# Optimization experiments

Measured on AMD Instinct MI355X. Metric: run time of the kernel, lower is better.

The kernel has to match this reference:

```python
import jax, jax.numpy as jnp
import numpy as np

EMBED_DIM = 1024
N1 = 4096
N2 = 4096


def setup_inputs() -> dict:
    key = jax.random.key(0)
    ks = jax.random.split(key, 14)
    s = 1.0 / np.sqrt(EMBED_DIM)
    def lin(k):
        kw, kb = jax.random.split(k)
        W = jax.random.uniform(kw, (EMBED_DIM, EMBED_DIM), jnp.float32, -s, s)
        b = jax.random.uniform(kb, (EMBED_DIM,), jnp.float32, -s, s)
        return W, b
    Wq1, bq1 = lin(ks[0]); Wk1, bk1 = lin(ks[1]); Wv1, bv1 = lin(ks[2])
    Wq2, bq2 = lin(ks[3]); Wk2, bk2 = lin(ks[4]); Wv2, bv2 = lin(ks[5])
    x1 = jax.random.normal(ks[6], (N1, EMBED_DIM), jnp.float32)
    x2 = jax.random.normal(ks[7], (N2, EMBED_DIM), jnp.float32)
    return {
        "input_tensor1": x1, "input_tensor2": x2,
        "Wq1": Wq1, "bq1": bq1, "Wk1": Wk1, "bk1": bk1, "Wv1": Wv1, "bv1": bv1,
        "Wq2": Wq2, "bq2": bq2, "Wk2": Wk2, "bk2": bk2, "Wv2": Wv2, "bv2": bv2,
    }


def reference(input_tensor1, input_tensor2,
              Wq1, bq1, Wk1, bk1, Wv1, bv1,
              Wq2, bq2, Wk2, bk2, Wv2, bv2):
    scale = 1.0 / jnp.sqrt(jnp.asarray(EMBED_DIM, input_tensor1.dtype))
    # torch Linear: y = x @ W.T + b
    q1 = input_tensor1 @ Wq1.T + bq1   # [N1, D]
    k1 = input_tensor1 @ Wk1.T + bk1
    v1 = input_tensor1 @ Wv1.T + bv1
    q2 = input_tensor2 @ Wq2.T + bq2   # [N2, D]
    k2 = input_tensor2 @ Wk2.T + bk2
    v2 = input_tensor2 @ Wv2.T + bv2
    # stream-2 queries attend over stream-1 keys/values
    scores1 = (q2 @ k1.T) * scale                  # [N2, N1]
    probs1 = jax.nn.softmax(scores1, axis=-1)      # dropout p=0 -> identity
    context1 = probs1 @ v1                         # [N2, D]
    # stream-1 queries attend over stream-2 keys/values
    scores2 = (q1 @ k2.T) * scale                  # [N1, N2]
    probs2 = jax.nn.softmax(scores2, axis=-1)
    context2 = probs2 @ v2                         # [N1, D]
    return (context1, context2)
```

## Files before the change

### kernel.cpp

```cpp
#include <hip/hip_runtime.h>
#include <hip/hip_bf16.h>
#include <cstdint>
#include <cstddef>

#define DEVINL __device__ __forceinline__

typedef __attribute__((ext_vector_type(4))) float   f32x4;
typedef __bf16 bf16x8 __attribute__((ext_vector_type(8)));
typedef __attribute__((ext_vector_type(4))) short   short4v;
typedef __attribute__((ext_vector_type(4))) float   float4v;

static constexpr int DIM = 1024;
static constexpr int NTOK = 4096;

DEVINL unsigned short f2bf(float f) {
  unsigned u = __float_as_uint(f);
  u += 0x7FFF + ((u >> 16) & 1);
  return (unsigned short)(u >> 16);
}
DEVINL float bf2f(unsigned short s) {
  return __uint_as_float(((unsigned)s) << 16);
}

DEVINL void gll16(const void* g, void* l) {
  __builtin_amdgcn_global_load_lds(
      (const __attribute__((address_space(1))) void*)g,
      (__attribute__((address_space(3))) void*)l, 16, 0, 0);
}

struct B3 { int bx, by, bz; };
DEVINL B3 xcd_remap(int GX, int GY, int GZ) {
  const int flat = blockIdx.x + GX * (blockIdx.y + GY * blockIdx.z);
  const int nwg  = GX * GY * GZ;
  const int chunk = nwg >> 3;
  const int vbid = (flat & 7) * chunk + (flat >> 3);
  B3 r;
  r.bx = vbid % GX;
  r.by = (vbid / GX) % GY;
  r.bz = vbid / (GX * GY);
  return r;
}

DEVINL void core256x128(const unsigned short* __restrict__ A, int lda,
                        const unsigned short* __restrict__ B, int ldb,
                        int K, int brow, int bcol, f32x4 acc[4][4])
{
  __shared__ unsigned short lds[24576];
  const int t = threadIdx.x;
  const int w = t >> 6, l = t & 63;
  const int wr = w >> 1, wc = w & 1;
  const int l15 = l & 15;
  const int scol = ((l & 3) ^ ((l >> 3) & 3)) << 3;
  const int cs = (((l >> 4) ^ ((l15 >> 1) & 3)) << 3);

  const unsigned short* aL = A + (size_t)(brow * 256 + (l >> 2)) * lda + scol;
  const unsigned short* bL = B + (size_t)(bcol * 128 + (l >> 2)) * ldb + scol;

#pragma unroll
  for (int m = 0; m < 4; ++m)
#pragma unroll
    for (int n = 0; n < 4; ++n) {
      f32x4 z = {0.f, 0.f, 0.f, 0.f};
      acc[m][n] = z;
    }

#define STAGE(buf, kt)                                                         \
  {                                                                            \
    gll16(aL + (size_t)(w * 16) * lda + (size_t)(kt) * 32,                     \
          lds + (buf) * 12288 + w * 512);                                      \
    gll16(aL + (size_t)(128 + w * 16) * lda + (size_t)(kt) * 32,               \
          lds + (buf) * 12288 + 4096 + w * 512);                               \
    gll16(bL + (size_t)(w * 16) * ldb + (size_t)(kt) * 32,                     \
          lds + (buf) * 12288 + 8192 + w * 512);                               \
  }

#define BARR() do { asm volatile("" ::: "memory");                             \
                    __builtin_amdgcn_s_barrier();                              \
                    asm volatile("" ::: "memory"); } while (0)

  const int NT = K >> 5;

  STAGE(0, 0);
  asm volatile("s_waitcnt vmcnt(0)" ::: "memory");
  BARR();

  bf16x8 af[4], bfv[4];
  for (int kt = 0; kt < NT; ++kt) {
    const int cur = kt & 1;
    if (kt + 1 < NT) STAGE(cur ^ 1, kt + 1);

#pragma unroll
    for (int m = 0; m < 4; ++m)
      af[m] = *(const bf16x8*)(lds + cur * 12288 + (wr * 64 + m * 16 + l15) * 32 + cs);
#pragma unroll
    for (int n = 0; n < 4; ++n)
      bfv[n] = *(const bf16x8*)(lds + cur * 12288 + 8192 + (wc * 64 + n * 16 + l15) * 32 + cs);

    __builtin_amdgcn_s_setprio(1);
#pragma unroll
    for (int m = 0; m < 4; ++m)
#pragma unroll
      for (int n = 0; n < 4; ++n)
        acc[m][n] = __builtin_amdgcn_mfma_f32_16x16x32_bf16(af[m], bfv[n], acc[m][n], 0, 0, 0);
    __builtin_amdgcn_s_setprio(0);

    asm volatile("s_waitcnt vmcnt(0)" ::: "memory");
    BARR();
  }
#undef STAGE
#undef BARR
}

__global__ __launch_bounds__(512, 4)
void gemm_scores(const unsigned short* __restrict__ A,
                 const unsigned short* __restrict__ B,
                 unsigned short* __restrict__ S, float scale)
{
  const B3 b = xcd_remap(32, 16, 1);
  f32x4 acc[4][4];
  core256x128(A, DIM, B, DIM, DIM, b.by, b.bx, acc);

  const int t = threadIdx.x, w = t >> 6, l = t & 63;
  const int wr = w >> 1, wc = w & 1;
  const int rr = (l >> 4) * 4, cc = l & 15;
#pragma unroll
  for (int m = 0; m < 4; ++m) {
    const int row0 = b.by * 256 + wr * 64 + m * 16 + rr;
#pragma unroll
    for (int n = 0; n < 4; ++n) {
      const int col = b.bx * 128 + wc * 64 + n * 16 + cc;
#pragma unroll
      for (int i = 0; i < 4; ++i)
        S[(size_t)(row0 + i) * NTOK + col] = f2bf(acc[m][n][i] * scale);
    }
  }
}

__global__ __launch_bounds__(512, 4)
void qkv_gemm(const unsigned short* __restrict__ x1, const unsigned short* __restrict__ x2,
              const unsigned short* __restrict__ W6,
              const float* bq1, const float* bk1, const float* bv1,
              const float* bq2, const float* bk2, const float* bv2,
              unsigned short* q1, unsigned short* k1, unsigned short* v1T,
              unsigned short* q2, unsigned short* k2, unsigned short* v2T)
{
  const B3 b = xcd_remap(8, 16, 6);
  const int g = b.bz;
  const unsigned short* A = (g < 3) ? x1 : x2;
  const unsigned short* W = W6 + (size_t)g * (DIM * DIM);
  const float* bias = (g == 0) ? bq1 : (g == 1) ? bk1 : (g == 2) ? bv1
                    : (g == 3) ? bq2 : (g == 4) ? bk2 : bv2;
  unsigned short* out = (g == 0) ? q1 : (g == 1) ? k1 : (g == 2) ? v1T
                      : (g == 3) ? q2 : (g == 4) ? k2 : v2T;
  const bool vT = (g == 2 || g == 5);

  f32x4 acc[4][4];
  core256x128(A, DIM, W, DIM, DIM, b.by, b.bx, acc);

  const int t = threadIdx.x, w = t >> 6, l = t & 63;
  const int wr = w >> 1, wc = w & 1;
  const int rr = (l >> 4) * 4, cc = l & 15;

  if (!vT) {
#pragma unroll
    for (int m = 0; m < 4; ++m) {
      const int row0 = b.by * 256 + wr * 64 + m * 16 + rr;
#pragma unroll
      for (int n = 0; n < 4; ++n) {
        const int col = b.bx * 128 + wc * 64 + n * 16 + cc;
        const float bv_ = bias[col];
#pragma unroll
        for (int i = 0; i < 4; ++i)
          out[(size_t)(row0 + i) * DIM + col] = f2bf(acc[m][n][i] + bv_);
      }
    }
  } else {
#pragma unroll
    for (int m = 0; m < 4; ++m) {
      const int row0 = b.by * 256 + wr * 64 + m * 16 + rr;
#pragma unroll
      for (int n = 0; n < 4; ++n) {
        const int col = b.bx * 128 + wc * 64 + n * 16 + cc;
        const float bv_ = bias[col];
        short4v pk;
#pragma unroll
        for (int i = 0; i < 4; ++i) pk[i] = (short)f2bf(acc[m][n][i] + bv_);
        *(short4v*)(out + (size_t)col * NTOK + row0) = pk;
      }
    }
  }
}

__global__ __launch_bounds__(512, 4)
void pv_gemm(const unsigned short* __restrict__ S1,
             const unsigned short* __restrict__ S2,
             const unsigned short* __restrict__ vTcat,
             float* __restrict__ out, float* __restrict__ P)
{
  const B3 b = xcd_remap(16, 16, 2);
  const int bx = b.bx, by = b.by, z = b.bz;
  const unsigned short* A = ((bx < 8) ? S1 : S2) + (size_t)z * 2048;
  const unsigned short* B = vTcat + (size_t)z * 2048;

  f32x4 acc[4][4];
  core256x128(A, NTOK, B, NTOK, 2048, by, bx, acc);

  const int t = threadIdx.x, w = t >> 6, l = t & 63;
  const int wr = w >> 1, wc = w & 1;
  const int rr = (l >> 4) * 4, cc = l & 15;
#pragma unroll
  for (int m = 0; m < 4; ++m) {
    const int row0 = by * 256 + wr * 64 + m * 16 + rr;
#pragma unroll
    for (int n = 0; n < 4; ++n) {
      const int cg = bx * 128 + wc * 64 + n * 16 + cc;
#pragma unroll
      for (int i = 0; i < 4; ++i) {
        const int r = row0 + i;
        if (z) {
          P[(size_t)r * 2048 + cg] = acc[m][n][i];
        } else {
          float* dst = (cg < 1024) ? (out + (size_t)r * 1024 + cg)
                                   : (out + 4194304 + (size_t)r * 1024 + (cg - 1024));
          *dst = acc[m][n][i];
        }
      }
    }
  }
}

__global__ __launch_bounds__(256)
void add_pv(float* __restrict__ out, const float* __restrict__ P)
{
  const int idx = blockIdx.x * 256 + threadIdx.x;
  const int r  = idx >> 9;
  const int c4 = (idx & 511) << 2;
  const float4v p = *(const float4v*)(P + (size_t)r * 2048 + c4);
  float* dst = (c4 < 1024) ? (out + (size_t)r * 1024 + c4)
                           : (out + 4194304 + (size_t)r * 1024 + (c4 - 1024));
  float4v a = *(const float4v*)dst;
#pragma unroll
  for (int j = 0; j < 4; ++j) a[j] += p[j];
  *(float4v*)dst = a;
}

__global__ __launch_bounds__(256)
void softmax_inplace(unsigned short* __restrict__ S)
{
  const int row = blockIdx.x;
  unsigned short* r = S + (size_t)row * NTOK;
  const int t = threadIdx.x, wave = t >> 6, lane = t & 63;
  __shared__ float red[4];

  bf16x8 d0 = *(const bf16x8*)(r + t * 8);
  bf16x8 d1 = *(const bf16x8*)(r + 2048 + t * 8);
  float v[16];
  {
    const unsigned short* p0 = (const unsigned short*)&d0;
    const unsigned short* p1 = (const unsigned short*)&d1;
#pragma unroll
    for (int j = 0; j < 8; ++j) { v[j] = bf2f(p0[j]); v[8 + j] = bf2f(p1[j]); }
  }
  float mx = v[0];
#pragma unroll
  for (int j = 1; j < 16; ++j) mx = fmaxf(mx, v[j]);
#pragma unroll
  for (int o = 32; o > 0; o >>= 1) mx = fmaxf(mx, __shfl_xor(mx, o));
  if (lane == 0) red[wave] = mx;
  __syncthreads();
  mx = fmaxf(fmaxf(red[0], red[1]), fmaxf(red[2], red[3]));

  float s = 0.f;
#pragma unroll
  for (int j = 0; j < 16; ++j) { v[j] = __expf(v[j] - mx); s += v[j]; }
#pragma unroll
  for (int o = 32; o > 0; o >>= 1) s += __shfl_xor(s, o);
  __syncthreads();
  if (lane == 0) red[wave] = s;
  __syncthreads();
  s = red[0] + red[1] + red[2] + red[3];
  const float inv = 1.0f / s;

  unsigned short o0[8], o1[8];
#pragma unroll
  for (int j = 0; j < 8; ++j) { o0[j] = f2bf(v[j] * inv); o1[j] = f2bf(v[8 + j] * inv); }
  *(bf16x8*)(r + t * 8)        = *(const bf16x8*)o0;
  *(bf16x8*)(r + 2048 + t * 8) = *(const bf16x8*)o1;
}

__global__ __launch_bounds__(256)
void cvt2(const float* __restrict__ a, const float* __restrict__ b,
          unsigned short* __restrict__ oa, unsigned short* __restrict__ ob)
{
  const float* in = blockIdx.y ? b : a;
  unsigned short* out = blockIdx.y ? ob : oa;
  const size_t i = ((size_t)blockIdx.x * 256 + threadIdx.x) * 4;
  float4v x = *(const float4v*)(in + i);
  short4v o;
#pragma unroll
  for (int j = 0; j < 4; ++j) o[j] = (short)f2bf(x[j]);
  *(short4v*)(out + i) = o;
}

__global__ __launch_bounds__(256)
void cvt_w(const float* w0, const float* w1, const float* w2,
           const float* w3, const float* w4, const float* w5,
           unsigned short* __restrict__ W6)
{
  const float* srcs[6] = {w0, w1, w2, w3, w4, w5};
  const float* in = srcs[blockIdx.y];
  unsigned short* out = W6 + (size_t)blockIdx.y * (DIM * DIM);
  const size_t i = ((size_t)blockIdx.x * 256 + threadIdx.x) * 4;
  float4v x = *(const float4v*)(in + i);
  short4v o;
#pragma unroll
  for (int j = 0; j < 4; ++j) o[j] = (short)f2bf(x[j]);
  *(short4v*)(out + i) = o;
}

extern "C" void kernel_launch(void* const* d_in, const int* in_sizes, int n_in,
                              void* d_out, int out_size, void* d_ws, size_t ws_size,
                              hipStream_t stream)
{
  const float* x1  = (const float*)d_in[0];
  const float* x2  = (const float*)d_in[1];
  const float* Wq1 = (const float*)d_in[2];  const float* bq1 = (const float*)d_in[3];
  const float* Wk1 = (const float*)d_in[4];  const float* bk1 = (const float*)d_in[5];
  const float* Wv1 = (const float*)d_in[6];  const float* bv1 = (const float*)d_in[7];
  const float* Wq2 = (const float*)d_in[8];  const float* bq2 = (const float*)d_in[9];
  const float* Wk2 = (const float*)d_in[10]; const float* bk2 = (const float*)d_in[11];
  const float* Wv2 = (const float*)d_in[12]; const float* bv2 = (const float*)d_in[13];
  float* out = (float*)d_out;

  unsigned short* ws  = (unsigned short*)d_ws;
  const size_t NTD = (size_t)NTOK * DIM;
  const size_t SM  = (size_t)NTOK * NTOK;
  unsigned short* x1b = ws;
  unsigned short* x2b = x1b + NTD;
  unsigned short* W6  = x2b + NTD;
  unsigned short* S1  = ws;
  unsigned short* S2  = ws + SM;
  unsigned short* q1  = ws + 2 * SM;
  unsigned short* k1  = q1 + NTD;
  unsigned short* q2  = k1 + NTD;
  unsigned short* k2  = q2 + NTD;
  unsigned short* vT  = k2 + NTD;
  unsigned short* v1T = vT;
  unsigned short* v2T = vT + NTD;
  float* P = (float*)q1;

  const dim3 blk(256);
  cvt2 <<<dim3(NTD / 1024, 2), blk, 0, stream>>>(x1, x2, x1b, x2b);
  cvt_w<<<dim3((DIM * DIM) / 1024, 6), blk, 0, stream>>>(Wq1, Wk1, Wv1, Wq2, Wk2, Wv2, W6);

  qkv_gemm<<<dim3(8, 16, 6), dim3(512), 0, stream>>>(
      x1b, x2b, W6, bq1, bk1, bv1, bq2, bk2, bv2, q1, k1, v1T, q2, k2, v2T);

  const float scale = 0.03125f;

  gemm_scores<<<dim3(32, 16), dim3(512), 0, stream>>>(q2, k1, S1, scale);
  softmax_inplace<<<dim3(NTOK), blk, 0, stream>>>(S1);
  gemm_scores<<<dim3(32, 16), dim3(512), 0, stream>>>(q1, k2, S2, scale);
  softmax_inplace<<<dim3(NTOK), blk, 0, stream>>>(S2);

  pv_gemm<<<dim3(16, 16, 2), dim3(512), 0, stream>>>(S1, S2, vT, out, P);
  add_pv<<<dim3(8192), blk, 0, stream>>>(out, P);
}
```

Before: 275.7 us.

## Deepen GEMM LDS pipeline to six buffers and drop split-K in PV GEMM

The shared GEMM core moves from double buffering to a six-slot LDS ring with four tiles prefetched ahead. It uses graded vmcnt waits and a single barrier per iteration, so global loads overlap more MFMA work. Launch bounds drop to 2 blocks per SM to fit the larger LDS footprint. The PV GEMM no longer splits K into two halves, which removes the partial-sum buffer and the separate add kernel. The cost is half as many PV blocks and lower occupancy.

Result: no change. 277.0 us (median of 2 runs) (+0.5%).

```diff
diff --git a/kernel.cpp b/kernel.cpp
--- a/kernel.cpp
+++ b/kernel.cpp
@@ -45,16 +45,16 @@
                         const unsigned short* __restrict__ B, int ldb,
                         int K, int brow, int bcol, f32x4 acc[4][4])
 {
-  __shared__ unsigned short lds[24576];
+  __shared__ unsigned short lds[73728];
   const int t = threadIdx.x;
   const int w = t >> 6, l = t & 63;
   const int wr = w >> 1, wc = w & 1;
   const int l15 = l & 15;
   const int scol = ((l & 3) ^ ((l >> 3) & 3)) << 3;
-  const int cs = (((l >> 4) ^ ((l15 >> 1) & 3)) << 3);
-
-  const unsigned short* aL = A + (size_t)(brow * 256 + (l >> 2)) * lda + scol;
-  const unsigned short* bL = B + (size_t)(bcol * 128 + (l >> 2)) * ldb + scol;
+  const int cs   = (((l >> 4) ^ ((l15 >> 1) & 3)) << 3);
+
+  const unsigned short* aL = A + (size_t)(brow * 256 + w * 16 + (l >> 2)) * lda + scol;
+  const unsigned short* bL = B + (size_t)(bcol * 128 + w * 16 + (l >> 2)) * ldb + scol;
 
 #pragma unroll
   for (int m = 0; m < 4; ++m)
@@ -66,35 +66,41 @@
 
 #define STAGE(buf, kt)                                                         \
   {                                                                            \
-    gll16(aL + (size_t)(w * 16) * lda + (size_t)(kt) * 32,                     \
+    gll16(aL + (size_t)(kt) * 32,                                              \
           lds + (buf) * 12288 + w * 512);                                      \
-    gll16(aL + (size_t)(128 + w * 16) * lda + (size_t)(kt) * 32,               \
+    gll16(aL + (size_t)128 * lda + (size_t)(kt) * 32,                          \
           lds + (buf) * 12288 + 4096 + w * 512);                               \
-    gll16(bL + (size_t)(w * 16) * ldb + (size_t)(kt) * 32,                     \
+    gll16(bL + (size_t)(kt) * 32,                                              \
           lds + (buf) * 12288 + 8192 + w * 512);                               \
   }
 
-#define BARR() do { asm volatile("" ::: "memory");                             \
-                    __builtin_amdgcn_s_barrier();                              \
-                    asm volatile("" ::: "memory"); } while (0)
-
   const int NT = K >> 5;
 
-  STAGE(0, 0);
-  asm volatile("s_waitcnt vmcnt(0)" ::: "memory");
-  BARR();
+  STAGE(0, 0); STAGE(1, 1); STAGE(2, 2); STAGE(3, 3);
 
   bf16x8 af[4], bfv[4];
+  int cur = 0;
   for (int kt = 0; kt < NT; ++kt) {
-    const int cur = kt & 1;
-    if (kt + 1 < NT) STAGE(cur ^ 1, kt + 1);
-
+    int st = cur + 4; if (st >= 6) st -= 6;
+    if (kt + 4 < NT) STAGE(st, kt + 4);
+
+    const int rem = NT - 1 - kt;
+    if (rem >= 4)      asm volatile("s_waitcnt vmcnt(12)" ::: "memory");
+    else if (rem == 3) asm volatile("s_waitcnt vmcnt(9)"  ::: "memory");
+    else if (rem == 2) asm volatile("s_waitcnt vmcnt(6)"  ::: "memory");
+    else if (rem == 1) asm volatile("s_waitcnt vmcnt(3)"  ::: "memory");
+    else               asm volatile("s_waitcnt vmcnt(0)"  ::: "memory");
+    asm volatile("" ::: "memory");
+    __builtin_amdgcn_s_barrier();
+    asm volatile("" ::: "memory");
+
+    const unsigned short* base = lds + cur * 12288;
 #pragma unroll
     for (int m = 0; m < 4; ++m)
-      af[m] = *(const bf16x8*)(lds + cur * 12288 + (wr * 64 + m * 16 + l15) * 32 + cs);
+      af[m] = *(const bf16x8*)(base + (wr * 64 + m * 16 + l15) * 32 + cs);
 #pragma unroll
     for (int n = 0; n < 4; ++n)
-      bfv[n] = *(const bf16x8*)(lds + cur * 12288 + 8192 + (wc * 64 + n * 16 + l15) * 32 + cs);
+      bfv[n] = *(const bf16x8*)(base + 8192 + (wc * 64 + n * 16 + l15) * 32 + cs);
 
     __builtin_amdgcn_s_setprio(1);
 #pragma unroll
@@ -104,14 +110,12 @@
         acc[m][n] = __builtin_amdgcn_mfma_f32_16x16x32_bf16(af[m], bfv[n], acc[m][n], 0, 0, 0);
     __builtin_amdgcn_s_setprio(0);
 
-    asm volatile("s_waitcnt vmcnt(0)" ::: "memory");
-    BARR();
+    cur = (cur + 1 == 6) ? 0 : cur + 1;
   }
 #undef STAGE
-#undef BARR
-}
-
-__global__ __launch_bounds__(512, 4)
+}
+
+__global__ __launch_bounds__(512, 2)
 void gemm_scores(const unsigned short* __restrict__ A,
                  const unsigned short* __restrict__ B,
                  unsigned short* __restrict__ S, float scale)
@@ -136,7 +140,7 @@
   }
 }
 
-__global__ __launch_bounds__(512, 4)
+__global__ __launch_bounds__(512, 2)
 void qkv_gemm(const unsigned short* __restrict__ x1, const unsigned short* __restrict__ x2,
               const unsigned short* __restrict__ W6,
               const float* bq1, const float* bk1, const float* bv1,
@@ -191,19 +195,18 @@
   }
 }
 
-__global__ __launch_bounds__(512, 4)
+__global__ __launch_bounds__(512, 2)
 void pv_gemm(const unsigned short* __restrict__ S1,
              const unsigned short* __restrict__ S2,
              const unsigned short* __restrict__ vTcat,
-             float* __restrict__ out, float* __restrict__ P)
-{
-  const B3 b = xcd_remap(16, 16, 2);
-  const int bx = b.bx, by = b.by, z = b.bz;
-  const unsigned short* A = ((bx < 8) ? S1 : S2) + (size_t)z * 2048;
-  const unsigned short* B = vTcat + (size_t)z * 2048;
+             float* __restrict__ out)
+{
+  const B3 b = xcd_remap(16, 16, 1);
+  const int bx = b.bx, by = b.by;
+  const unsigned short* A = (bx < 8) ? S1 : S2;
 
   f32x4 acc[4][4];
-  core256x128(A, NTOK, B, NTOK, 2048, by, bx, acc);
+  core256x128(A, NTOK, vTcat, NTOK, NTOK, by, bx, acc);
 
   const int t = threadIdx.x, w = t >> 6, l = t & 63;
   const int wr = w >> 1, wc = w & 1;
@@ -214,34 +217,12 @@
 #pragma unroll
     for (int n = 0; n < 4; ++n) {
       const int cg = bx * 128 + wc * 64 + n * 16 + cc;
-#pragma unroll
-      for (int i = 0; i < 4; ++i) {
-        const int r = row0 + i;
-        if (z) {
-          P[(size_t)r * 2048 + cg] = acc[m][n][i];
-        } else {
-          float* dst = (cg < 1024) ? (out + (size_t)r * 1024 + cg)
-                                   : (out + 4194304 + (size_t)r * 1024 + (cg - 1024));
-          *dst = acc[m][n][i];
-        }
-      }
-    }
-  }
-}
-
-__global__ __launch_bounds__(256)
-void add_pv(float* __restrict__ out, const float* __restrict__ P)
-{
-  const int idx = blockIdx.x * 256 + threadIdx.x;
-  const int r  = idx >> 9;
-  const int c4 = (idx & 511) << 2;
-  const float4v p = *(const float4v*)(P + (size_t)r * 2048 + c4);
-  float* dst = (c4 < 1024) ? (out + (size_t)r * 1024 + c4)
-                           : (out + 4194304 + (size_t)r * 1024 + (c4 - 1024));
-  float4v a = *(const float4v*)dst;
-#pragma unroll
-  for (int j = 0; j < 4; ++j) a[j] += p[j];
-  *(float4v*)dst = a;
+      float* dstBase = (cg < 1024) ? (out + cg) : (out + 4194304 + (cg - 1024));
+#pragma unroll
+      for (int i = 0; i < 4; ++i)
+        dstBase[(size_t)(row0 + i) * 1024] = acc[m][n][i];
+    }
+  }
 }
 
 __global__ __launch_bounds__(256)
@@ -347,7 +328,6 @@
   unsigned short* vT  = k2 + NTD;
   unsigned short* v1T = vT;
   unsigned short* v2T = vT + NTD;
-  float* P = (float*)q1;
 
   const dim3 blk(256);
   cvt2 <<<dim3(NTD / 1024, 2), blk, 0, stream>>>(x1, x2, x1b, x2b);
@@ -363,6 +343,5 @@
   gemm_scores<<<dim3(32, 16), dim3(512), 0, stream>>>(q1, k2, S2, scale);
   softmax_inplace<<<dim3(NTOK), blk, 0, stream>>>(S2);
 
-  pv_gemm<<<dim3(16, 16, 2), dim3(512), 0, stream>>>(S1, S2, vT, out, P);
-  add_pv<<<dim3(8192), blk, 0, stream>>>(out, P);
-}
+  pv_gemm<<<dim3(16, 16), dim3(512), 0, stream>>>(S1, S2, vT, out);
+}
```

## Use 256x256 GEMM tiles with a four-buffer, three-stage-ahead load pipeline

Applied to the files above, without the earlier changes.

Replaces the 256x128 GEMM core with a 256x256 tile core. Each wave now covers a 128x64 sub-tile (8x4 MFMAs), which raises data reuse per LDS load. The double-buffered loop, which drained all loads with vmcnt(0) on every iteration, becomes a 4-slot ring buffer that prefetches three K-steps ahead and uses partial vmcnt waits. The cost is 128KB of LDS and more accumulator registers per block, so occupancy drops to one block per CU. Grids also halve, leaving fewer blocks than CUs for the scores and PV GEMMs.

Result: faster. 270.0 us (-2.1%).

```diff
diff --git a/kernel.cpp b/kernel.cpp
--- a/kernel.cpp
+++ b/kernel.cpp
@@ -41,23 +41,23 @@
   return r;
 }
 
-DEVINL void core256x128(const unsigned short* __restrict__ A, int lda,
-                        const unsigned short* __restrict__ B, int ldb,
-                        int K, int brow, int bcol, f32x4 acc[4][4])
-{
-  __shared__ unsigned short lds[24576];
+DEVINL void core256sq(const unsigned short* __restrict__ A, int lda,
+                      const unsigned short* __restrict__ B, int ldb,
+                      int K, int brow, int bcol, f32x4 acc[8][4])
+{
+  __shared__ unsigned short lds[65536];
   const int t = threadIdx.x;
   const int w = t >> 6, l = t & 63;
-  const int wr = w >> 1, wc = w & 1;
+  const int wr = w >> 2, wc = w & 3;
   const int l15 = l & 15;
   const int scol = ((l & 3) ^ ((l >> 3) & 3)) << 3;
-  const int cs = (((l >> 4) ^ ((l15 >> 1) & 3)) << 3);
-
-  const unsigned short* aL = A + (size_t)(brow * 256 + (l >> 2)) * lda + scol;
-  const unsigned short* bL = B + (size_t)(bcol * 128 + (l >> 2)) * ldb + scol;
-
-#pragma unroll
-  for (int m = 0; m < 4; ++m)
+  const int cs   = (((l >> 4) ^ ((l15 >> 1) & 3)) << 3);
+
+  const unsigned short* aL = A + (size_t)(brow * 256 + w * 16 + (l >> 2)) * lda + scol;
+  const unsigned short* bL = B + (size_t)(bcol * 256 + w * 16 + (l >> 2)) * ldb + scol;
+
+#pragma unroll
+  for (int m = 0; m < 8; ++m)
 #pragma unroll
     for (int n = 0; n < 4; ++n) {
       f32x4 z = {0.f, 0.f, 0.f, 0.f};
@@ -66,69 +66,69 @@
 
 #define STAGE(buf, kt)                                                         \
   {                                                                            \
-    gll16(aL + (size_t)(w * 16) * lda + (size_t)(kt) * 32,                     \
-          lds + (buf) * 12288 + w * 512);                                      \
-    gll16(aL + (size_t)(128 + w * 16) * lda + (size_t)(kt) * 32,               \
-          lds + (buf) * 12288 + 4096 + w * 512);                               \
-    gll16(bL + (size_t)(w * 16) * ldb + (size_t)(kt) * 32,                     \
-          lds + (buf) * 12288 + 8192 + w * 512);                               \
-  }
-
-#define BARR() do { asm volatile("" ::: "memory");                             \
-                    __builtin_amdgcn_s_barrier();                              \
-                    asm volatile("" ::: "memory"); } while (0)
+    gll16(aL + (size_t)(kt) * 32,                                              \
+          lds + (buf) * 16384 + w * 512);                                      \
+    gll16(aL + (size_t)128 * lda + (size_t)(kt) * 32,                          \
+          lds + (buf) * 16384 + 4096 + w * 512);                               \
+    gll16(bL + (size_t)(kt) * 32,                                              \
+          lds + (buf) * 16384 + 8192 + w * 512);                               \
+    gll16(bL + (size_t)128 * ldb + (size_t)(kt) * 32,                          \
+          lds + (buf) * 16384 + 12288 + w * 512);                              \
+  }
 
   const int NT = K >> 5;
 
-  STAGE(0, 0);
-  asm volatile("s_waitcnt vmcnt(0)" ::: "memory");
-  BARR();
-
-  bf16x8 af[4], bfv[4];
+  STAGE(0, 0); STAGE(1, 1); STAGE(2, 2);
+
+  bf16x8 af[8], bfv[4];
   for (int kt = 0; kt < NT; ++kt) {
-    const int cur = kt & 1;
-    if (kt + 1 < NT) STAGE(cur ^ 1, kt + 1);
-
-#pragma unroll
-    for (int m = 0; m < 4; ++m)
-      af[m] = *(const bf16x8*)(lds + cur * 12288 + (wr * 64 + m * 16 + l15) * 32 + cs);
+    const int rem = NT - 1 - kt;
+    if (rem >= 2)      asm volatile("s_waitcnt vmcnt(8)" ::: "memory");
+    else if (rem == 1) asm volatile("s_waitcnt vmcnt(4)" ::: "memory");
+    else               asm volatile("s_waitcnt vmcnt(0)" ::: "memory");
+    asm volatile("" ::: "memory");
+    __builtin_amdgcn_s_barrier();
+    asm volatile("" ::: "memory");
+
+    if (kt + 3 < NT) STAGE((kt + 3) & 3, kt + 3);
+
+    const unsigned short* base = lds + (kt & 3) * 16384;
+#pragma unroll
+    for (int m = 0; m < 8; ++m)
+      af[m] = *(const bf16x8*)(base + (wr * 128 + m * 16 + l15) * 32 + cs);
 #pragma unroll
     for (int n = 0; n < 4; ++n)
-      bfv[n] = *(const bf16x8*)(lds + cur * 12288 + 8192 + (wc * 64 + n * 16 + l15) * 32 + cs);
+      bfv[n] = *(const bf16x8*)(base + 8192 + (wc * 64 + n * 16 + l15) * 32 + cs);
 
     __builtin_amdgcn_s_setprio(1);
 #pragma unroll
-    for (int m = 0; m < 4; ++m)
+    for (int m = 0; m < 8; ++m)
 #pragma unroll
       for (int n = 0; n < 4; ++n)
         acc[m][n] = __builtin_amdgcn_mfma_f32_16x16x32_bf16(af[m], bfv[n], acc[m][n], 0, 0, 0);
     __builtin_amdgcn_s_setprio(0);
-
-    asm volatile("s_waitcnt vmcnt(0)" ::: "memory");
-    BARR();
   }
 #undef STAGE
-#undef BARR
-}
-
-__global__ __launch_bounds__(512, 4)
+}
+
+__global__ __launch_bounds__(512, 1)
 void gemm_scores(const unsigned short* __restrict__ A,
                  const unsigned short* __restrict__ B,
                  unsigned short* __restrict__ S, float scale)
 {
-  const B3 b = xcd_remap(32, 16, 1);
-  f32x4 acc[4][4];
-  core256x128(A, DIM, B, DIM, DIM, b.by, b.bx, acc);
+  const B3 b = xcd_remap(16, 16, 1);
+  f32x4 acc[8][4];
+  core256sq(A, DIM, B, DIM, DIM, b.by, b.bx, acc);
 
   const int t = threadIdx.x, w = t >> 6, l = t & 63;
-  const int wr = w >> 1, wc = w & 1;
+  const int wr = w >> 2, wc = w & 3;
   const int rr = (l >> 4) * 4, cc = l & 15;
 #pragma unroll
-  for (int m = 0; m < 4; ++m) {
-    const int row0 = b.by * 256 + wr * 64 + m * 16 + rr;
+  for (int m = 0; m < 8; ++m) {
+    const int row0 = b.by * 256 + wr * 128 + m * 16 + rr;
 #pragma unroll
     for (int n = 0; n < 4; ++n) {
-      const int col = b.bx * 128 + wc * 64 + n * 16 + cc;
+      const int col = b.bx * 256 + wc * 64 + n * 16 + cc;
 #pragma unroll
       for (int i = 0; i < 4; ++i)
         S[(size_t)(row0 + i) * NTOK + col] = f2bf(acc[m][n][i] * scale);
@@ -136,7 +136,7 @@
   }
 }
 
-__global__ __launch_bounds__(512, 4)
+__global__ __launch_bounds__(512, 1)
 void qkv_gemm(const unsigned short* __restrict__ x1, const unsigned short* __restrict__ x2,
               const unsigned short* __restrict__ W6,
               const float* bq1, const float* bk1, const float* bv1,
@@ -144,7 +144,7 @@
               unsigned short* q1, unsigned short* k1, unsigned short* v1T,
               unsigned short* q2, unsigned short* k2, unsigned short* v2T)
 {
-  const B3 b = xcd_remap(8, 16, 6);
+  const B3 b = xcd_remap(4, 16, 6);
   const int g = b.bz;
   const unsigned short* A = (g < 3) ? x1 : x2;
   const unsigned short* W = W6 + (size_t)g * (DIM * DIM);
@@ -154,20 +154,20 @@
                       : (g == 3) ? q2 : (g == 4) ? k2 : v2T;
   const bool vT = (g == 2 || g == 5);
 
-  f32x4 acc[4][4];
-  core256x128(A, DIM, W, DIM, DIM, b.by, b.bx, acc);
+  f32x4 acc[8][4];
+  core256sq(A, DIM, W, DIM, DIM, b.by, b.bx, acc);
 
   const int t = threadIdx.x, w = t >> 6, l = t & 63;
-  const int wr = w >> 1, wc = w & 1;
+  const int wr = w >> 2, wc = w & 3;
   const int rr = (l >> 4) * 4, cc = l & 15;
 
   if (!vT) {
 #pragma unroll
-    for (int m = 0; m < 4; ++m) {
-      const int row0 = b.by * 256 + wr * 64 + m * 16 + rr;
+    for (int m = 0; m < 8; ++m) {
+      const int row0 = b.by * 256 + wr * 128 + m * 16 + rr;
 #pragma unroll
       for (int n = 0; n < 4; ++n) {
-        const int col = b.bx * 128 + wc * 64 + n * 16 + cc;
+        const int col = b.bx * 256 + wc * 64 + n * 16 + cc;
         const float bv_ = bias[col];
 #pragma unroll
         for (int i = 0; i < 4; ++i)
@@ -176,11 +176,11 @@
     }
   } else {
 #pragma unroll
-    for (int m = 0; m < 4; ++m) {
-      const int row0 = b.by * 256 + wr * 64 + m * 16 + rr;
+    for (int m = 0; m < 8; ++m) {
+      const int row0 = b.by * 256 + wr * 128 + m * 16 + rr;
 #pragma unroll
       for (int n = 0; n < 4; ++n) {
-        const int col = b.bx * 128 + wc * 64 + n * 16 + cc;
+        const int col = b.bx * 256 + wc * 64 + n * 16 + cc;
         const float bv_ = bias[col];
         short4v pk;
 #pragma unroll
@@ -191,29 +191,29 @@
   }
 }
 
-__global__ __launch_bounds__(512, 4)
+__global__ __launch_bounds__(512, 1)
 void pv_gemm(const unsigned short* __restrict__ S1,
              const unsigned short* __restrict__ S2,
              const unsigned short* __restrict__ vTcat,
              float* __restrict__ out, float* __restrict__ P)
 {
-  const B3 b = xcd_remap(16, 16, 2);
+  const B3 b = xcd_remap(8, 16, 2);
   const int bx = b.bx, by = b.by, z = b.bz;
-  const unsigned short* A = ((bx < 8) ? S1 : S2) + (size_t)z * 2048;
+  const unsigned short* A = ((bx < 4) ? S1 : S2) + (size_t)z * 2048;
   const unsigned short* B = vTcat + (size_t)z * 2048;
 
-  f32x4 acc[4][4];
-  core256x128(A, NTOK, B, NTOK, 2048, by, bx, acc);
+  f32x4 acc[8][4];
+  core256sq(A, NTOK, B, NTOK, 2048, by, bx, acc);
 
   const int t = threadIdx.x, w = t >> 6, l = t & 63;
-  const int wr = w >> 1, wc = w & 1;
+  const int wr = w >> 2, wc = w & 3;
   const int rr = (l >> 4) * 4, cc = l & 15;
 #pragma unroll
-  for (int m = 0; m < 4; ++m) {
-    const int row0 = by * 256 + wr * 64 + m * 16 + rr;
+  for (int m = 0; m < 8; ++m) {
+    const int row0 = by * 256 + wr * 128 + m * 16 + rr;
 #pragma unroll
     for (int n = 0; n < 4; ++n) {
-      const int cg = bx * 128 + wc * 64 + n * 16 + cc;
+      const int cg = bx * 256 + wc * 64 + n * 16 + cc;
 #pragma unroll
       for (int i = 0; i < 4; ++i) {
         const int r = row0 + i;
@@ -353,16 +353,16 @@
   cvt2 <<<dim3(NTD / 1024, 2), blk, 0, stream>>>(x1, x2, x1b, x2b);
   cvt_w<<<dim3((DIM * DIM) / 1024, 6), blk, 0, stream>>>(Wq1, Wk1, Wv1, Wq2, Wk2, Wv2, W6);
 
-  qkv_gemm<<<dim3(8, 16, 6), dim3(512), 0, stream>>>(
+  qkv_gemm<<<dim3(4, 16, 6), dim3(512), 0, stream>>>(
       x1b, x2b, W6, bq1, bk1, bv1, bq2, bk2, bv2, q1, k1, v1T, q2, k2, v2T);
 
   const float scale = 0.03125f;
 
-  gemm_scores<<<dim3(32, 16), dim3(512), 0, stream>>>(q2, k1, S1, scale);
+  gemm_scores<<<dim3(16, 16), dim3(512), 0, stream>>>(q2, k1, S1, scale);
   softmax_inplace<<<dim3(NTOK), blk, 0, stream>>>(S1);
-  gemm_scores<<<dim3(32, 16), dim3(512), 0, stream>>>(q1, k2, S2, scale);
+  gemm_scores<<<dim3(16, 16), dim3(512), 0, stream>>>(q1, k2, S2, scale);
   softmax_inplace<<<dim3(NTOK), blk, 0, stream>>>(S2);
 
-  pv_gemm<<<dim3(16, 16, 2), dim3(512), 0, stream>>>(S1, S2, vT, out, P);
+  pv_gemm<<<dim3(8, 16, 2), dim3(512), 0, stream>>>(S1, S2, vT, out, P);
   add_pv<<<dim3(8192), blk, 0, stream>>>(out, P);
 }
```
